# Performance work log

Measured on AMD Instinct MI355X. Metric: run time of the kernel, lower is better.

The kernel has to match this reference:

```python
import jax, jax.numpy as jnp
import numpy as np

D1 = 512
D2 = 1024  # = 2*D1 (concat of x1,y1 along channels)
B, S = 4, 2048


def _self_attn(x, Wq, bq, Wk, bk, Wv, bv):
    # Linear layers use torch convention: out = x @ W.T + b
    q = jnp.einsum('bsd,ed->bse', x, Wq) + bq
    k = jnp.einsum('bsd,ed->bse', x, Wk) + bk
    v = jnp.einsum('bsd,ed->bse', x, Wv) + bv
    # NOTE: original module has no 1/sqrt(d) scaling — keep it faithful.
    scores = jnp.einsum('bqe,bke->bqk', q, k)  # [B,S,S]
    attn = jax.nn.softmax(scores, axis=-1)
    return jnp.einsum('bqk,bke->bqe', attn, v)


def setup_inputs() -> dict:
    key = jax.random.key(0)
    ks = jax.random.split(key, 18)
    s1 = 1.0 / np.sqrt(D1)
    s2 = 1.0 / np.sqrt(D2)
    return {
        'x': jax.random.normal(ks[0], (B, S, D1), jnp.float32),
        'y': jax.random.normal(ks[1], (B, S, D1), jnp.float32),
        'sa1_Wq': jax.random.normal(ks[2], (D1, D1), jnp.float32) * s1,
        'sa1_bq': jnp.zeros((D1,), jnp.float32),
        'sa1_Wk': jax.random.normal(ks[3], (D1, D1), jnp.float32) * s1,
        'sa1_bk': jnp.zeros((D1,), jnp.float32),
        'sa1_Wv': jax.random.normal(ks[4], (D1, D1), jnp.float32) * s1,
        'sa1_bv': jnp.zeros((D1,), jnp.float32),
        'sa2_Wq': jax.random.normal(ks[5], (D2, D2), jnp.float32) * s2,
        'sa2_bq': jnp.zeros((D2,), jnp.float32),
        'sa2_Wk': jax.random.normal(ks[6], (D2, D2), jnp.float32) * s2,
        'sa2_bk': jnp.zeros((D2,), jnp.float32),
        'sa2_Wv': jax.random.normal(ks[7], (D2, D2), jnp.float32) * s2,
        'sa2_bv': jnp.zeros((D2,), jnp.float32),
        'weight1': jnp.ones((1,), jnp.float32),
        'weight2': jnp.ones((1,), jnp.float32),
    }


def reference(x, y, sa1_Wq, sa1_bq, sa1_Wk, sa1_bk, sa1_Wv, sa1_bv,
              sa2_Wq, sa2_bq, sa2_Wk, sa2_bk, sa2_Wv, sa2_bv,
              weight1, weight2):
    x1 = _self_attn(x, sa1_Wq, sa1_bq, sa1_Wk, sa1_bk, sa1_Wv, sa1_bv)
    x1 = x1 + y * weight2
    y1 = _self_attn(y, sa1_Wq, sa1_bq, sa1_Wk, sa1_bk, sa1_Wv, sa1_bv)
    y1 = y1 + x * weight1
    temp = jnp.concatenate((x1, y1), axis=2)  # [B,S,2*D1]
    return _self_attn(temp, sa2_Wq, sa2_bq, sa2_Wk, sa2_bk, sa2_Wv, sa2_bv)
```

## Files before the change

kernel.cpp:

```cpp
#include <hip/hip_runtime.h>
#include <hip/hip_bf16.h>
#include <cstdint>
#include <cstddef>


typedef __bf16 bf16;
typedef __attribute__((ext_vector_type(8))) __bf16 bf16x8;
typedef __attribute__((ext_vector_type(4))) __bf16 bf16x4;
typedef __attribute__((ext_vector_type(4))) float f32x4;

__device__ __forceinline__ void gld16(const bf16* g, bf16* s) {
    __builtin_amdgcn_global_load_lds(
        (const __attribute__((address_space(1))) void*)g,
        (__attribute__((address_space(3))) void*)s, 16, 0, 0);
}

#define WAIT_VM8   __builtin_amdgcn_s_waitcnt(8 | (7 << 4) | (0xF << 8))
#define WAIT_VM0   __builtin_amdgcn_s_waitcnt(0 | (7 << 4) | (0xF << 8))
#define WAIT_LGKM0 __builtin_amdgcn_s_waitcnt(0xF | (7 << 4) | (0 << 8) | (3 << 14))

__device__ __forceinline__ int swz(int row, int g) {
    return row * 64 + ((g ^ (row & 7)) << 3);
}

__global__ __launch_bounds__(256) void gemm_split(
    const bf16* __restrict__ A, long lda, long psA, long bsA,
    const bf16* __restrict__ B, long ldb, long psB, long bsB,
    void* __restrict__ C, long ldc, long psC, long bsC, int mode,
    const float* __restrict__ bias, const float* __restrict__ bias2, int nsplit,
    const float* __restrict__ resid, long ldr, long bsR,
    const float* __restrict__ scale,
    int K, int split, int nx, int ny, int nz)
{
    __shared__ __align__(16) bf16 As[2][128 * 64];
    __shared__ __align__(16) bf16 Bs[2][128 * 64];

    const int t    = threadIdx.x;
    const int wave = t >> 6;
    const int lane = t & 63;
    const int wr   = wave >> 1;
    const int wc   = wave & 1;
    const int r16  = lane & 15;
    const int quad = lane >> 4;

    const int g    = blockIdx.x;
    const int xcd  = g & 7;
    const int tk   = g >> 3;
    const int nst8 = gridDim.x >> 7;
    const int st   = xcd * nst8 + (tk >> 4);
    const int p    = tk & 15;
    const int snx  = nx >> 2, sny = ny >> 2;
    const int spz  = snx * sny;
    const int zz   = st / spz;
    const int rS   = st - zz * spz;
    const int sy   = rS / snx;
    const int sx   = rS - sy * snx;
    const int yb   = sy * 4 + (p >> 2);
    const int xb   = sx * 4 + (p & 3);

    const int  kh   = zz / nz;
    const long z    = zz - (long)kh * nz;
    const long kOff = (long)kh * K;

    const long row0 = (long)yb * 128;
    const long col0 = (long)xb * 128;

    const int srow = (lane >> 3);
    const int scol = ((lane & 7) ^ srow) * 8;

    const int ktiles = K >> 6;
    const int T = split * ktiles;

    const bf16* Az = A + z * bsA;
    const bf16* Bz = B + z * bsB;

    auto prefetch = [&](int ti, int buf) {
        const int ph = ti / ktiles;
        const int kt = (ti - ph * ktiles) << 6;
        const bf16* Ab = Az + (ph == 1 ? psA : 0);
        const bf16* Bb = Bz + (ph == 2 ? psB : 0);
#pragma unroll
        for (int p2 = 0; p2 < 4; ++p2) {
            const int chunk = wave * 32 + p2 * 8;
            gld16(Ab + (row0 + chunk + srow) * lda + kt + kOff + scol, &As[buf][chunk * 64]);
            gld16(Bb + (col0 + chunk + srow) * ldb + kt + kOff + scol, &Bs[buf][chunk * 64]);
        }
    };

    f32x4 acc[4][4];
#pragma unroll
    for (int r = 0; r < 4; ++r)
#pragma unroll
        for (int c = 0; c < 4; ++c)
            acc[r][c] = (f32x4){0.f, 0.f, 0.f, 0.f};

    prefetch(0, 0);
    prefetch(1, 1);
    for (int ti = 0; ti < T; ++ti) {
        const int cur = ti & 1;
        if (ti + 1 < T) WAIT_VM8; else WAIT_VM0;
        __builtin_amdgcn_s_barrier();
        bf16x8 af[2][4], bg[2][4];
#pragma unroll
        for (int kk = 0; kk < 2; ++kk) {
            const int g0 = (kk << 2) + quad;
#pragma unroll
            for (int r = 0; r < 4; ++r)
                af[kk][r] = *reinterpret_cast<const bf16x8*>(&As[cur][swz(wr * 64 + r * 16 + r16, g0)]);
#pragma unroll
            for (int c = 0; c < 4; ++c)
                bg[kk][c] = *reinterpret_cast<const bf16x8*>(&Bs[cur][swz(wc * 64 + c * 16 + r16, g0)]);
        }
        WAIT_LGKM0;
        __builtin_amdgcn_s_barrier();
        if (ti + 2 < T) prefetch(ti + 2, cur);
#pragma unroll
        for (int kk = 0; kk < 2; ++kk)
#pragma unroll
            for (int r = 0; r < 4; ++r)
#pragma unroll
                for (int c = 0; c < 4; ++c)
                    acc[r][c] = __builtin_amdgcn_mfma_f32_16x16x32_bf16(af[kk][r], bg[kk][c], acc[r][c], 0, 0, 0);
    }

    const float scv = resid ? *scale : 0.f;

#pragma unroll
    for (int r = 0; r < 4; ++r) {
#pragma unroll
        for (int c = 0; c < 4; ++c) {
            long gcol = col0 + wc * 64 + c * 16 + r16;
            float bv = 0.f;
            if (bias) bv = (gcol < nsplit) ? bias[gcol] : bias2[gcol - nsplit];
#pragma unroll
            for (int i = 0; i < 4; ++i) {
                long grow = row0 + wr * 64 + r * 16 + quad * 4 + i;
                float val = acc[r][c][i] + bv;
                if (mode == 0) {
                    if (resid) val += resid[z * bsR + grow * ldr + gcol] * scv;
                    ((float*)C)[z * bsC + grow * ldc + gcol] = val;
                } else if (mode == 1) {
                    if (resid) val += resid[z * bsR + grow * ldr + gcol] * scv;
                    bf16* Cb = (bf16*)C + z * bsC;
                    bf16 h = (bf16)val;
                    Cb[grow * ldc + gcol] = h;
                    Cb[psC + grow * ldc + gcol] = (bf16)(val - (float)h);
                } else if (mode == 3) {
                    ((float*)C)[(long)kh * psC + z * bsC + grow * ldc + gcol] = val;
                } else {
                    long b = grow >> 11, s = grow & 2047;
                    bf16* Cb = (bf16*)C + b * bsC;
                    bf16 h = (bf16)val;
                    Cb[gcol * ldc + s] = h;
                    Cb[psC + gcol * ldc + s] = (bf16)(val - (float)h);
                }
            }
        }
    }
}

__global__ __launch_bounds__(512) void gemm256(
    const bf16* __restrict__ A, long lda, long psA, long bsA,
    const bf16* __restrict__ B, long ldb, long psB, long bsB,
    void* __restrict__ C, long ldc, long psC, long bsC, int mode,
    const float* __restrict__ bias, const float* __restrict__ bias2, int nsplit,
    int K, int split, int nx, int ny)
{
    __shared__ __align__(16) bf16 As[2][256 * 64];
    __shared__ __align__(16) bf16 Bs[2][256 * 64];

    const int t    = threadIdx.x;
    const int wave = t >> 6;
    const int lane = t & 63;
    const int wm   = wave >> 2;
    const int wn   = wave & 3;
    const int r16  = lane & 15;
    const int quad = lane >> 4;

    const int g     = blockIdx.x;
    const int chunk = gridDim.x >> 3;
    const int idx   = (g & 7) * chunk + (g >> 3);
    const int tpz   = nx * ny;
    const int z     = idx / tpz;
    const int r0i   = idx - z * tpz;
    const int ty    = r0i / nx;
    const int tx    = r0i - ty * nx;
    const long row0 = (long)ty * 256;
    const long col0 = (long)tx * 256;

    const int srow = lane >> 3;
    const int scol = ((lane & 7) ^ srow) * 8;

    const int ktiles = K >> 6;
    const int T = split * ktiles;

    const bf16* Az = A + (long)z * bsA;
    const bf16* Bz = B + (long)z * bsB;

    auto prefetch = [&](int ti, int buf) {
        const int ph = ti / ktiles;
        const int kt = (ti - ph * ktiles) << 6;
        const bf16* Ab = Az + (ph == 1 ? psA : 0);
        const bf16* Bb = Bz + (ph == 2 ? psB : 0);
#pragma unroll
        for (int p2 = 0; p2 < 4; ++p2) {
            const int chnk = wave * 32 + p2 * 8;
            gld16(Ab + (row0 + chnk + srow) * lda + kt + scol, &As[buf][chnk * 64]);
            gld16(Bb + (col0 + chnk + srow) * ldb + kt + scol, &Bs[buf][chnk * 64]);
        }
    };

    f32x4 acc[8][4];
#pragma unroll
    for (int r = 0; r < 8; ++r)
#pragma unroll
        for (int c = 0; c < 4; ++c)
            acc[r][c] = (f32x4){0.f, 0.f, 0.f, 0.f};

    bf16x8 fA0[8], fB0[4], fA1[8], fB1[4];

    auto rdset0 = [&](int cur, int kk) {
        const int g0 = (kk << 2) + quad;
#pragma unroll
        for (int r = 0; r < 8; ++r)
            fA0[r] = *reinterpret_cast<const bf16x8*>(
                &As[cur][swz(wm * 128 + r * 16 + r16, g0)]);
#pragma unroll
        for (int c = 0; c < 4; ++c)
            fB0[c] = *reinterpret_cast<const bf16x8*>(
                &Bs[cur][swz(wn * 64 + c * 16 + r16, g0)]);
    };
    auto rdset1 = [&](int cur, int kk) {
        const int g0 = (kk << 2) + quad;
#pragma unroll
        for (int r = 0; r < 8; ++r)
            fA1[r] = *reinterpret_cast<const bf16x8*>(
                &As[cur][swz(wm * 128 + r * 16 + r16, g0)]);
#pragma unroll
        for (int c = 0; c < 4; ++c)
            fB1[c] = *reinterpret_cast<const bf16x8*>(
                &Bs[cur][swz(wn * 64 + c * 16 + r16, g0)]);
    };

    prefetch(0, 0);
    prefetch(1, 1);
    WAIT_VM8;
    __builtin_amdgcn_s_barrier();
    rdset0(0, 0);

    for (int ti = 0; ti < T; ++ti) {
        const int cur = ti & 1;

        rdset1(cur, 1);
        __builtin_amdgcn_sched_barrier(0);
        __builtin_amdgcn_s_setprio(1);
#pragma unroll
        for (int r = 0; r < 8; ++r)
#pragma unroll
            for (int c = 0; c < 4; ++c)
                acc[r][c] = __builtin_amdgcn_mfma_f32_16x16x32_bf16(
                    fA0[r], fB0[c], acc[r][c], 0, 0, 0);
        __builtin_amdgcn_s_setprio(0);
        __builtin_amdgcn_sched_barrier(0);

        WAIT_LGKM0;
        __builtin_amdgcn_s_barrier();
        if (ti + 2 < T) prefetch(ti + 2, cur);
        if (ti + 1 < T) {
            if (ti + 2 < T) WAIT_VM8; else WAIT_VM0;
            __builtin_amdgcn_s_barrier();
            rdset0(cur ^ 1, 0);
        }
        __builtin_amdgcn_sched_barrier(0);
        __builtin_amdgcn_s_setprio(1);
#pragma unroll
        for (int r = 0; r < 8; ++r)
#pragma unroll
            for (int c = 0; c < 4; ++c)
                acc[r][c] = __builtin_amdgcn_mfma_f32_16x16x32_bf16(
                    fA1[r], fB1[c], acc[r][c], 0, 0, 0);
        __builtin_amdgcn_s_setprio(0);
    }

#pragma unroll
    for (int r = 0; r < 8; ++r) {
#pragma unroll
        for (int c = 0; c < 4; ++c) {
            const long gcol = col0 + wn * 64 + c * 16 + r16;
            float bv = 0.f;
            if (bias) bv = (gcol < nsplit) ? bias[gcol] : bias2[gcol - nsplit];
#pragma unroll
            for (int i = 0; i < 4; ++i) {
                const long grow = row0 + wm * 128 + r * 16 + quad * 4 + i;
                float val = acc[r][c][i] + bv;
                if (mode == 0) {
                    ((float*)C)[(long)z * bsC + grow * ldc + gcol] = val;
                } else {
                    bf16* Cb = (bf16*)C + (long)z * bsC;
                    bf16 h = (bf16)val;
                    Cb[grow * ldc + gcol] = h;
                    Cb[psC + grow * ldc + gcol] = (bf16)(val - (float)h);
                }
            }
        }
    }
}

__global__ __launch_bounds__(256) void reduce_pv(
    const float* __restrict__ p0, const float* __restrict__ p1,
    const float* __restrict__ resid, const float* __restrict__ scale,
    bf16* __restrict__ outp, long psC)
{
    const long gid = (long)blockIdx.x * 256 + threadIdx.x;
    const long f4  = gid * 4;
    const long z   = f4 >> 20;
    const long rem = f4 & ((1L << 20) - 1);
    const long row = rem >> 9;
    const long col = rem & 511;
    const float scv = *scale;
    f32x4 a = *reinterpret_cast<const f32x4*>(p0 + f4);
    f32x4 b = *reinterpret_cast<const f32x4*>(p1 + f4);
    f32x4 r = *reinterpret_cast<const f32x4*>(resid + f4);
    bf16x4 h, l;
#pragma unroll
    for (int j = 0; j < 4; ++j) {
        float v = a[j] + b[j] + r[j] * scv;
        h[j] = (bf16)v;
        l[j] = (bf16)(v - (float)h[j]);
    }
    bf16* dst = outp + z * (2048L * 1024) + row * 1024 + col;
    *reinterpret_cast<bf16x4*>(dst) = h;
    *reinterpret_cast<bf16x4*>(dst + psC) = l;
}

__global__ __launch_bounds__(256) void softmax_planes(float* __restrict__ S)
{
    __shared__ float redm[4], reds[4];
    float* srow = S + (long)blockIdx.x * 2048;
    const int t = threadIdx.x;
    const int lane = t & 63;
    const int wave = t >> 6;

    f32x4 v0 = *reinterpret_cast<const f32x4*>(srow + t * 4);
    f32x4 v1 = *reinterpret_cast<const f32x4*>(srow + 1024 + t * 4);

    float m = v0[0];
#pragma unroll
    for (int i = 1; i < 4; ++i) m = fmaxf(m, v0[i]);
#pragma unroll
    for (int i = 0; i < 4; ++i) m = fmaxf(m, v1[i]);
#pragma unroll
    for (int off = 32; off > 0; off >>= 1) m = fmaxf(m, __shfl_xor(m, off));
    if (lane == 0) redm[wave] = m;
    __syncthreads();
    m = fmaxf(fmaxf(redm[0], redm[1]), fmaxf(redm[2], redm[3]));

    float s = 0.f;
#pragma unroll
    for (int i = 0; i < 4; ++i) { v0[i] = __expf(v0[i] - m); s += v0[i]; }
#pragma unroll
    for (int i = 0; i < 4; ++i) { v1[i] = __expf(v1[i] - m); s += v1[i]; }
#pragma unroll
    for (int off = 32; off > 0; off >>= 1) s += __shfl_xor(s, off);
    if (lane == 0) reds[wave] = s;
    __syncthreads();
    s = reds[0] + reds[1] + reds[2] + reds[3];
    float inv = 1.f / s;

    bf16x4 h0, h1, l0, l1;
#pragma unroll
    for (int i = 0; i < 4; ++i) {
        float a = v0[i] * inv, b = v1[i] * inv;
        h0[i] = (bf16)a; l0[i] = (bf16)(a - (float)h0[i]);
        h1[i] = (bf16)b; l1[i] = (bf16)(b - (float)h1[i]);
    }
    bf16* ph = (bf16*)srow;
    *reinterpret_cast<bf16x4*>(ph + t * 4) = h0;
    *reinterpret_cast<bf16x4*>(ph + 1024 + t * 4) = h1;
    *reinterpret_cast<bf16x4*>(ph + 2048 + t * 4) = l0;
    *reinterpret_cast<bf16x4*>(ph + 3072 + t * 4) = l1;
}

__global__ __launch_bounds__(256) void split2_f32(
    const float* __restrict__ in, bf16* __restrict__ hi, bf16* __restrict__ lo)
{
    long i = ((long)blockIdx.x * 256 + threadIdx.x) * 4;
    f32x4 v = *reinterpret_cast<const f32x4*>(in + i);
    bf16x4 h, l;
#pragma unroll
    for (int j = 0; j < 4; ++j) {
        h[j] = (bf16)v[j];
        l[j] = (bf16)(v[j] - (float)h[j]);
    }
    *reinterpret_cast<bf16x4*>(hi + i) = h;
    *reinterpret_cast<bf16x4*>(lo + i) = l;
}

extern "C" void kernel_launch(void* const* d_in, const int* in_sizes, int n_in,
                              void* d_out, int out_size, void* d_ws, size_t ws_size,
                              hipStream_t stream)
{
    const float* x   = (const float*)d_in[0];
    const float* y   = (const float*)d_in[1];
    const float* Wq1 = (const float*)d_in[2];
    const float* bq1 = (const float*)d_in[3];
    const float* Wk1 = (const float*)d_in[4];
    const float* bk1 = (const float*)d_in[5];
    const float* Wv1 = (const float*)d_in[6];
    const float* bv1 = (const float*)d_in[7];
    const float* Wq2 = (const float*)d_in[8];
    const float* bq2 = (const float*)d_in[9];
    const float* Wk2 = (const float*)d_in[10];
    const float* bk2 = (const float*)d_in[11];
    const float* Wv2 = (const float*)d_in[12];
    const float* bv2 = (const float*)d_in[13];
    const float* w1  = (const float*)d_in[14];
    const float* w2  = (const float*)d_in[15];
    float* out = (float*)d_out;

    const size_t MB = 1ull << 20;
    char* ws = (char*)d_ws;
    const long S = 2048, M4 = 8192, E1 = 512, E2 = 1024;
    const long W1ps = E1 * E1, W2ps = E2 * E2;

    const int cfg = (ws_size >= 207 * MB) ? 2 : 0;

    auto gemm = [&](const bf16* A, long lda, long psA, long bsA,
                    const bf16* B, long ldb, long psB, long bsB,
                    void* C, long ldc, long psC, long bsC, int mode,
                    const float* bias, const float* bias2, int nsplit,
                    const float* resid, long ldr, long bsR,
                    const float* scale, int M, int N, int K, int split,
                    int gz, int nz) {
        int nx = N / 128, ny = M / 128;
        dim3 g((unsigned)(nx * ny * gz));
        gemm_split<<<g, dim3(256), 0, stream>>>(
            A, lda, psA, bsA, B, ldb, psB, bsB, C, ldc, psC, bsC, mode,
            bias, bias2, nsplit, resid, ldr, bsR, scale, K, split, nx, ny, nz);
    };
    auto g256 = [&](const bf16* A, long lda, long psA, long bsA,
                    const bf16* B, long ldb, long psB, long bsB,
                    void* C, long ldc, long psC, long bsC, int mode,
                    const float* bias, const float* bias2, int nsplit,
                    int K, int split, int M, int N, int gz) {
        int nx = N / 256, ny = M / 256;
        gemm256<<<dim3((unsigned)(nx * ny * gz)), dim3(512), 0, stream>>>(
            A, lda, psA, bsA, B, ldb, psB, bsB, C, ldc, psC, bsC, mode,
            bias, bias2, nsplit, K, split, nx, ny);
    };
    auto conv2 = [&](const float* in, bf16* hi, bf16* lo, long n) {
        split2_f32<<<dim3((unsigned)(n / 1024)), dim3(256), 0, stream>>>(in, hi, lo);
    };

    if (cfg == 2) {
        bf16* xyp   = (bf16*)d_out;
        bf16* Wqk1p = (bf16*)(ws + 0 * MB);
        bf16* Wv1p  = (bf16*)(ws + 2 * MB);
        bf16* Wqk2p = (bf16*)(ws + 3 * MB);
        bf16* Wv2p  = (bf16*)(ws + 11 * MB);
        bf16* temp  = (bf16*)(ws + 15 * MB);
        bf16* qk    = (bf16*)(ws + 47 * MB);
        bf16* vt    = (bf16*)(ws + 111 * MB);
        float* Sc   = (float*)(ws + 143 * MB);

        const long PXY = 16384L * 512;
        const long PW1 = 1024L * 512;
        const long PW2 = 2048L * 1024;
        const long PQ1 = 16384L * 1024;
        const long PQ2 = 8192L * 2048;
        const long PT  = 8192L * 1024;
        const long BV1 = 2 * E1 * S;
        const long BV2 = 2 * E2 * S;
        const long PVH = 4L * 2048 * 512;
        float* pvScr = (float*)d_out;

        conv2(x, xyp, xyp + PXY, M4 * E1);
        conv2(y, xyp + M4 * E1, xyp + PXY + M4 * E1, M4 * E1);
        conv2(Wq1, Wqk1p, Wqk1p + PW1, W1ps);
        conv2(Wk1, Wqk1p + W1ps, Wqk1p + PW1 + W1ps, W1ps);
        conv2(Wv1, Wv1p, Wv1p + W1ps, W1ps);
        conv2(Wq2, Wqk2p, Wqk2p + PW2, W2ps);
        conv2(Wk2, Wqk2p + W2ps, Wqk2p + PW2 + W2ps, W2ps);
        conv2(Wv2, Wv2p, Wv2p + W2ps, W2ps);

        g256(xyp, E1, PXY, 0, Wqk1p, E1, PW1, 0,
             qk, 1024, PQ1, 0, 1, bq1, bk1, 512,
             512, 3, 16384, 1024, 1);
        gemm(xyp, E1, PXY, 0, Wv1p, E1, W1ps, 0,
             vt, S, E1 * S, BV1, 2, bv1, nullptr, 512,
             nullptr, 0, 0, nullptr, 16384, 512, 512, 3, 1, 1);

        g256(qk, 1024, PQ1, S * 1024, qk + 512, 1024, PQ1, S * 1024,
             Sc, S, 0, S * S, 0, nullptr, nullptr, 0, 512, 3, 2048, 2048, 4);
        softmax_planes<<<dim3(8192), dim3(256), 0, stream>>>(Sc);
        gemm((const bf16*)Sc, 4096, 2048, S * 4096, vt, S, E1 * S, BV1,
             pvScr, 512, PVH, 2048L * 512, 3, nullptr, nullptr, 0,
             nullptr, 0, 0, nullptr, 2048, 512, 1024, 3, 8, 4);
        reduce_pv<<<dim3(4096), dim3(256), 0, stream>>>(
            pvScr, pvScr + PVH, y, w2, temp, PT);

        g256(qk + M4 * 1024, 1024, PQ1, S * 1024,
             qk + M4 * 1024 + 512, 1024, PQ1, S * 1024,
             Sc, S, 0, S * S, 0, nullptr, nullptr, 0, 512, 3, 2048, 2048, 4);
        softmax_planes<<<dim3(8192), dim3(256), 0, stream>>>(Sc);
        gemm((const bf16*)Sc, 4096, 2048, S * 4096, vt + 4 * BV1, S, E1 * S, BV1,
             pvScr, 512, PVH, 2048L * 512, 3, nullptr, nullptr, 0,
             nullptr, 0, 0, nullptr, 2048, 512, 1024, 3, 8, 4);
        reduce_pv<<<dim3(4096), dim3(256), 0, stream>>>(
            pvScr, pvScr + PVH, x, w1, temp + 512, PT);

        g256(temp, E2, PT, 0, Wqk2p, E2, PW2, 0,
             qk, 2048, PQ2, 0, 1, bq2, bk2, 1024,
             1024, 3, 8192, 2048, 1);
        gemm(temp, E2, PT, 0, Wv2p, E2, W2ps, 0,
             vt, S, E2 * S, BV2, 2, bv2, nullptr, 1024,
             nullptr, 0, 0, nullptr, 8192, 1024, 1024, 1, 1, 1);
        g256(qk, 2048, PQ2, S * 2048, qk + 1024, 2048, PQ2, S * 2048,
             Sc, S, 0, S * S, 0, nullptr, nullptr, 0, 1024, 3, 2048, 2048, 4);
        softmax_planes<<<dim3(8192), dim3(256), 0, stream>>>(Sc);
        gemm((const bf16*)Sc, 4096, 2048, S * 4096, vt, S, E2 * S, BV2,
             out, E2, 0, S * E2, 0, nullptr, nullptr, 1024,
             nullptr, 0, 0, nullptr, 2048, 1024, 2048, 1, 4, 4);
    } else {
        bf16* xp = (bf16*)d_out;
        bf16* yp = xp + 2 * M4 * E1;
        bf16* Wq1p = (bf16*)(ws + 0 * MB);
        bf16* Wk1p = (bf16*)(ws + 1 * MB);
        bf16* Wv1p = (bf16*)(ws + 2 * MB);
        bf16* temp = (bf16*)(ws + 3 * MB);
        bf16* qb   = (bf16*)(ws + 35 * MB);
        bf16* kb   = (bf16*)(ws + 43 * MB);
        bf16* vt   = (bf16*)(ws + 51 * MB);
        float* Sc  = (float*)(ws + 59 * MB);
        bf16* Wq2p = (bf16*)d_out;
        bf16* Wk2p = Wq2p + 2 * W2ps;
        bf16* Wv2p = Wk2p + 2 * W2ps;

        conv2(x, xp, xp + M4 * E1, M4 * E1);
        conv2(y, yp, yp + M4 * E1, M4 * E1);
        conv2(Wq1, Wq1p, Wq1p + W1ps, W1ps);
        conv2(Wk1, Wk1p, Wk1p + W1ps, W1ps);
        conv2(Wv1, Wv1p, Wv1p + W1ps, W1ps);

        auto stage1 = [&](const bf16* sp, const float* resid, const float* scale, long colOff) {
            for (int b = 0; b < 4; ++b) {
                const bf16* sb = sp + (long)b * S * E1;
                gemm(sb, E1, M4 * E1, 0, Wq1p, E1, W1ps, 0, qb, E1, S * E1, 0, 1,
                     bq1, nullptr, 512, nullptr, 0, 0, nullptr, 2048, 512, 512, 3, 1, 1);
                gemm(sb, E1, M4 * E1, 0, Wk1p, E1, W1ps, 0, kb, E1, S * E1, 0, 1,
                     bk1, nullptr, 512, nullptr, 0, 0, nullptr, 2048, 512, 512, 3, 1, 1);
                gemm(sb, E1, M4 * E1, 0, Wv1p, E1, W1ps, 0, vt, S, E1 * S, 0, 2,
                     bv1, nullptr, 512, nullptr, 0, 0, nullptr, 2048, 512, 512, 3, 1, 1);
                gemm(qb, E1, S * E1, 0, kb, E1, S * E1, 0, Sc, S, 0, 0, 0,
                     nullptr, nullptr, 2048, nullptr, 0, 0, nullptr, 2048, 2048, 512, 3, 1, 1);
                softmax_planes<<<dim3(2048), dim3(256), 0, stream>>>(Sc);
                gemm((const bf16*)Sc, 4096, 2048, 0, vt, S, E1 * S, 0,
                     temp + colOff + (long)b * S * 1024, 1024, M4 * 1024, 0, 1,
                     nullptr, nullptr, 512, resid + (long)b * S * E1, E1, 0, scale,
                     2048, 512, 2048, 3, 1, 1);
            }
        };

        stage1(xp, y, w2, 0);
        stage1(yp, x, w1, 512);

        conv2(Wq2, Wq2p, Wq2p + W2ps, W2ps);
        conv2(Wk2, Wk2p, Wk2p + W2ps, W2ps);
        conv2(Wv2, Wv2p, Wv2p + W2ps, W2ps);

        for (int b = 0; b < 4; ++b) {
            const bf16* tb = temp + (long)b * S * E2;
            gemm(tb, E2, M4 * E2, 0, Wq2p, E2, W2ps, 0, qb, E2, S * E2, 0, 1,
                 bq2, nullptr, 1024, nullptr, 0, 0, nullptr, 2048, 1024, 1024, 3, 1, 1);
            gemm(tb, E2, M4 * E2, 0, Wk2p, E2, W2ps, 0, kb, E2, S * E2, 0, 1,
                 bk2, nullptr, 1024, nullptr, 0, 0, nullptr, 2048, 1024, 1024, 3, 1, 1);
            gemm(tb, E2, M4 * E2, 0, Wv2p, E2, W2ps, 0, vt, S, E2 * S, 0, 2,
                 bv2, nullptr, 1024, nullptr, 0, 0, nullptr, 2048, 1024, 1024, 1, 1, 1);
            gemm(qb, E2, S * E2, 0, kb, E2, S * E2, 0, Sc, S, 0, 0, 0,
                 nullptr, nullptr, 2048, nullptr, 0, 0, nullptr, 2048, 2048, 1024, 3, 1, 1);
            softmax_planes<<<dim3(2048), dim3(256), 0, stream>>>(Sc);
            gemm((const bf16*)Sc, 4096, 2048, 0, vt, S, E2 * S, 0,
                 out + (long)b * S * E2, E2, 0, 0, 0, nullptr, nullptr, 1024,
                 nullptr, 0, 0, nullptr, 2048, 1024, 2048, 1, 1, 1);
        }
    }

    (void)in_sizes; (void)n_in; (void)out_size;
}
```

Baseline: 880.6 us.

## Switch gemm256 to 32x32x16 MFMA with whole-tile LDS fragment loads

Replaces the 16x16x32 MFMA tiling in the 256x256 GEMM kernel with 32x32x16 MFMAs (4x2 accumulator tiles of 16 floats per wave). The pipeline changes: each k-tile now loads all A/B fragments for the full 64-wide K slice at once instead of double-buffering half-tile register sets, then splits the MFMA work into two halves around the prefetch barrier. The larger MFMA shape cuts LDS reads per flop and instruction count, at the cost of more live registers for fragments and less overlap between LDS reads and MFMAs. The epilogue row/column mapping is updated for the 32x32 output layout.

```diff
diff --git a/kernel.cpp b/kernel.cpp
--- a/kernel.cpp
+++ b/kernel.cpp
@@ -8,6 +8,7 @@
 typedef __attribute__((ext_vector_type(8))) __bf16 bf16x8;
 typedef __attribute__((ext_vector_type(4))) __bf16 bf16x4;
 typedef __attribute__((ext_vector_type(4))) float f32x4;
+typedef __attribute__((ext_vector_type(16))) float f32x16;
 
 __device__ __forceinline__ void gld16(const bf16* g, bf16* s) {
     __builtin_amdgcn_global_load_lds(
@@ -174,8 +175,8 @@
     const int lane = t & 63;
     const int wm   = wave >> 2;
     const int wn   = wave & 3;
-    const int r16  = lane & 15;
-    const int quad = lane >> 4;
+    const int l31  = lane & 31;
+    const int half = lane >> 5;
 
     const int g     = blockIdx.x;
     const int chunk = gridDim.x >> 3;
@@ -210,89 +211,84 @@
         }
     };
 
-    f32x4 acc[8][4];
-#pragma unroll
-    for (int r = 0; r < 8; ++r)
-#pragma unroll
-        for (int c = 0; c < 4; ++c)
-            acc[r][c] = (f32x4){0.f, 0.f, 0.f, 0.f};
-
-    bf16x8 fA0[8], fB0[4], fA1[8], fB1[4];
-
-    auto rdset0 = [&](int cur, int kk) {
-        const int g0 = (kk << 2) + quad;
-#pragma unroll
-        for (int r = 0; r < 8; ++r)
-            fA0[r] = *reinterpret_cast<const bf16x8*>(
-                &As[cur][swz(wm * 128 + r * 16 + r16, g0)]);
-#pragma unroll
-        for (int c = 0; c < 4; ++c)
-            fB0[c] = *reinterpret_cast<const bf16x8*>(
-                &Bs[cur][swz(wn * 64 + c * 16 + r16, g0)]);
-    };
-    auto rdset1 = [&](int cur, int kk) {
-        const int g0 = (kk << 2) + quad;
-#pragma unroll
-        for (int r = 0; r < 8; ++r)
-            fA1[r] = *reinterpret_cast<const bf16x8*>(
-                &As[cur][swz(wm * 128 + r * 16 + r16, g0)]);
-#pragma unroll
-        for (int c = 0; c < 4; ++c)
-            fB1[c] = *reinterpret_cast<const bf16x8*>(
-                &Bs[cur][swz(wn * 64 + c * 16 + r16, g0)]);
-    };
+    f32x16 acc[4][2];
+#pragma unroll
+    for (int m = 0; m < 4; ++m)
+#pragma unroll
+        for (int n = 0; n < 2; ++n)
+#pragma unroll
+            for (int i = 0; i < 16; ++i)
+                acc[m][n][i] = 0.f;
 
     prefetch(0, 0);
     prefetch(1, 1);
-    WAIT_VM8;
-    __builtin_amdgcn_s_barrier();
-    rdset0(0, 0);
-
     for (int ti = 0; ti < T; ++ti) {
         const int cur = ti & 1;
-
-        rdset1(cur, 1);
+        if (ti + 1 < T) WAIT_VM8; else WAIT_VM0;
+        __builtin_amdgcn_s_barrier();
+
+        bf16x8 af[4][4], bg[2][4];
+#pragma unroll
+        for (int mt = 0; mt < 2; ++mt)
+#pragma unroll
+            for (int ks = 0; ks < 4; ++ks)
+                af[mt][ks] = *reinterpret_cast<const bf16x8*>(
+                    &As[cur][swz(wm * 128 + mt * 32 + l31, ks * 2 + half)]);
+#pragma unroll
+        for (int ks = 0; ks < 4; ++ks)
+            bg[0][ks] = *reinterpret_cast<const bf16x8*>(
+                &Bs[cur][swz(wn * 64 + l31, ks * 2 + half)]);
+#pragma unroll
+        for (int ks = 0; ks < 4; ++ks)
+            bg[1][ks] = *reinterpret_cast<const bf16x8*>(
+                &Bs[cur][swz(wn * 64 + 32 + l31, ks * 2 + half)]);
+#pragma unroll
+        for (int mt = 2; mt < 4; ++mt)
+#pragma unroll
+            for (int ks = 0; ks < 4; ++ks)
+                af[mt][ks] = *reinterpret_cast<const bf16x8*>(
+                    &As[cur][swz(wm * 128 + mt * 32 + l31, ks * 2 + half)]);
+
+        __builtin_amdgcn_s_setprio(1);
+#pragma unroll
+        for (int ks = 0; ks < 4; ++ks)
+#pragma unroll
+            for (int mt = 0; mt < 2; ++mt)
+#pragma unroll
+                for (int nt = 0; nt < 2; ++nt)
+                    acc[mt][nt] = __builtin_amdgcn_mfma_f32_32x32x16_bf16(
+                        af[mt][ks], bg[nt][ks], acc[mt][nt], 0, 0, 0);
+        __builtin_amdgcn_s_setprio(0);
+
         __builtin_amdgcn_sched_barrier(0);
-        __builtin_amdgcn_s_setprio(1);
-#pragma unroll
-        for (int r = 0; r < 8; ++r)
-#pragma unroll
-            for (int c = 0; c < 4; ++c)
-                acc[r][c] = __builtin_amdgcn_mfma_f32_16x16x32_bf16(
-                    fA0[r], fB0[c], acc[r][c], 0, 0, 0);
-        __builtin_amdgcn_s_setprio(0);
-        __builtin_amdgcn_sched_barrier(0);
-
         WAIT_LGKM0;
         __builtin_amdgcn_s_barrier();
         if (ti + 2 < T) prefetch(ti + 2, cur);
-        if (ti + 1 < T) {
-            if (ti + 2 < T) WAIT_VM8; else WAIT_VM0;
-            __builtin_amdgcn_s_barrier();
-            rdset0(cur ^ 1, 0);
-        }
-        __builtin_amdgcn_sched_barrier(0);
+
         __builtin_amdgcn_s_setprio(1);
 #pragma unroll
-        for (int r = 0; r < 8; ++r)
-#pragma unroll
-            for (int c = 0; c < 4; ++c)
-                acc[r][c] = __builtin_amdgcn_mfma_f32_16x16x32_bf16(
-                    fA1[r], fB1[c], acc[r][c], 0, 0, 0);
+        for (int ks = 0; ks < 4; ++ks)
+#pragma unroll
+            for (int mt = 2; mt < 4; ++mt)
+#pragma unroll
+                for (int nt = 0; nt < 2; ++nt)
+                    acc[mt][nt] = __builtin_amdgcn_mfma_f32_32x32x16_bf16(
+                        af[mt][ks], bg[nt][ks], acc[mt][nt], 0, 0, 0);
         __builtin_amdgcn_s_setprio(0);
     }
 
 #pragma unroll
-    for (int r = 0; r < 8; ++r) {
-#pragma unroll
-        for (int c = 0; c < 4; ++c) {
-            const long gcol = col0 + wn * 64 + c * 16 + r16;
+    for (int mt = 0; mt < 4; ++mt) {
+#pragma unroll
+        for (int nt = 0; nt < 2; ++nt) {
+            const long gcol = col0 + wn * 64 + nt * 32 + l31;
             float bv = 0.f;
             if (bias) bv = (gcol < nsplit) ? bias[gcol] : bias2[gcol - nsplit];
 #pragma unroll
-            for (int i = 0; i < 4; ++i) {
-                const long grow = row0 + wm * 128 + r * 16 + quad * 4 + i;
-                float val = acc[r][c][i] + bv;
+            for (int i = 0; i < 16; ++i) {
+                const long grow = row0 + wm * 128 + mt * 32
+                                + (i & 3) + 8 * (i >> 2) + 4 * half;
+                float val = acc[mt][nt][i] + bv;
                 if (mode == 0) {
                     ((float*)C)[(long)z * bsC + grow * ldc + gcol] = val;
                 } else {
```

Measured after the change: 875.6 us. About the same (-0.6%).
